# Kernel tuning notes

Measured on AMD Instinct MI355X. Metric: run time of the kernel, lower is better.

The kernel has to match this reference:

```python
import jax, jax.numpy as jnp
import numpy as np

B, T = 128, 100
DZ, DA, DU, K, DOBS, H = 64, 32, 8, 8, 16, 128
JITTER = 1e-4  # _safe_cholesky: sym + jitter*I, then first try adds 1.0*jitter*I again


def setup_inputs() -> dict:
    key = jax.random.key(0)
    ks = jax.random.split(key, 10)
    eye_z = jnp.eye(DZ, dtype=jnp.float32)
    # stable-ish per-component transition matrices
    A_mats = 0.9 * eye_z[None] + 0.05 * jax.random.normal(ks[0], (K, DZ, DZ), jnp.float32)
    B_mats = 0.1 * jax.random.normal(ks[1], (K, DZ, DU), jnp.float32)
    C_mats = 0.3 * jax.random.normal(ks[2], (K, DA, DZ), jnp.float32)
    a_seq = jax.random.normal(ks[3], (B, T, DA), jnp.float32)
    h_obs = jax.random.normal(ks[4], (B, DOBS), jnp.float32)
    u_seq = jax.random.normal(ks[5], (B, T, DU), jnp.float32)
    mask = jnp.ones((B, T), jnp.float32)
    a_0 = jnp.zeros((1, DA), jnp.float32)          # nn.Parameter a_0
    P_0 = 10.0 * eye_z                              # 10 * eye(dim_z)
    Q = 0.05 * eye_z                                # Q_std * eye(dim_z)
    R = 0.05 * jnp.eye(DA, dtype=jnp.float32)       # R_std * eye(dim_a)
    din = DA + DOBS + DU
    s = 1.0 / float(np.sqrt(H))
    W_ih = s * jax.random.normal(ks[6], (3 * H, din), jnp.float32)
    W_hh = s * jax.random.normal(ks[7], (3 * H, H), jnp.float32)
    b_ih = jnp.zeros((3 * H,), jnp.float32)
    b_hh = jnp.zeros((3 * H,), jnp.float32)
    W_out = s * jax.random.normal(ks[8], (K, H), jnp.float32)
    b_out = jnp.zeros((K,), jnp.float32)
    return dict(a_seq=a_seq, h_obs=h_obs, u_seq=u_seq, mask=mask,
                A_mats=A_mats, B_mats=B_mats, C_mats=C_mats,
                a_0=a_0, P_0=P_0, Q=Q, R=R,
                W_ih=W_ih, W_hh=W_hh, b_ih=b_ih, b_hh=b_hh,
                W_out=W_out, b_out=b_out, epoch=100)


def _sym(M):
    return 0.5 * (M + jnp.swapaxes(M, -1, -2))


def _gru_alpha(x, h, W_ih, W_hh, b_ih, b_hh, W_out, b_out):
    # GRU-cell alpha_net: mixture weights over K components
    gi = x @ W_ih.T + b_ih
    gh = h @ W_hh.T + b_hh
    ir, iz, inn = jnp.split(gi, 3, axis=-1)
    hr, hz, hn = jnp.split(gh, 3, axis=-1)
    r = jax.nn.sigmoid(ir + hr)
    zg = jax.nn.sigmoid(iz + hz)
    n = jnp.tanh(inn + r * hn)
    h_new = (1.0 - zg) * n + zg * h
    alpha = jax.nn.softmax(h_new @ W_out.T + b_out, axis=-1)
    return alpha, h_new


def _kalman_forward(a_seq, h_obs, u_seq, mask, A_mats, B_mats, C_mats,
                    a_0, P_0, Q, R, W_ih, W_hh, b_ih, b_hh, W_out, b_out):
    Bsz = a_seq.shape[0]
    I = jnp.eye(DZ, dtype=a_seq.dtype)

    def mix(alpha):
        A = jnp.einsum('bk,kij->bij', alpha, A_mats)
        Bc = jnp.einsum('bk,kij->bij', alpha, B_mats)
        C = jnp.einsum('bk,kij->bij', alpha, C_mats)
        return A, Bc, C

    def alpha_net(a, u, h):
        x = jnp.concatenate([a, h_obs, u], axis=-1)
        return _gru_alpha(x, h, W_ih, W_hh, b_ih, b_hh, W_out, b_out)

    gru_h = jnp.zeros((Bsz, H), a_seq.dtype)
    a_prev = jnp.broadcast_to(a_0, (Bsz, DA))
    alpha0, gru_h = alpha_net(a_prev, u_seq[:, 0], gru_h)
    A_k0, B_k0, C_k0 = mix(alpha0)

    z0 = jnp.zeros((Bsz, DZ), a_seq.dtype)
    P0 = jnp.broadcast_to(P_0, (Bsz, DZ, DZ))

    def step(carry, inp):
        z_prev, P, h, A_k, B_k, C_k = carry
        a_k, u_k, m_k = inp  # [B,da], [B,du], [B]
        mk = m_k[:, None]
        # predict with matrices chosen at previous step
        z = jnp.einsum('bij,bj->bi', A_k, z_prev) + jnp.einsum('bij,bj->bi', B_k, u_k)
        a_hat = jnp.einsum('bij,bj->bi', C_k, z)
        r_k = a_k - a_hat
        CP = jnp.einsum('bij,bjk->bik', C_k, P)                      # C P
        S = jnp.einsum('bik,bjk->bij', CP, C_k) + R                   # C P C^T + R
        # K = solve(S^T, C P^T)^T  (i.e. K = P C^T S^{-1})
        CPt = jnp.einsum('bij,bkj->bik', C_k, P)
        Kg = jnp.swapaxes(jnp.linalg.solve(jnp.swapaxes(S, -1, -2), CPt), -1, -2)
        Kg = Kg * m_k[:, None, None]
        IKC = I - jnp.einsum('bij,bjk->bik', Kg, C_k)
        # Joseph form update
        P_filt = (jnp.einsum('bij,bjk,blk->bil', IKC, P, IKC)
                  + jnp.einsum('bij,jk,blk->bil', Kg, R, Kg))
        P_filt = _sym(P_filt)
        z_mean = z + jnp.einsum('bij,bj->bi', Kg, r_k)
        L = jnp.linalg.cholesky(_sym(P_filt) + 2.0 * JITTER * I)      # safe cholesky
        z_filt = z_mean                                               # dist.mean
        a_filt = jnp.einsum('bij,bj->bi', C_k, z_filt)
        a_k_hat = mk * a_k + (1.0 - mk) * a_filt
        C_old = C_k
        alpha, h = alpha_net(a_k_hat, u_k, h)
        A_n, B_n, C_n = mix(alpha)
        z_pred = (jnp.einsum('bij,bj->bi', A_n, z_filt)
                  + jnp.einsum('bij,bj->bi', B_n, u_k))
        a_pred = jnp.einsum('bij,bj->bi', C_n, z_pred)
        P_pred = _sym(jnp.einsum('bij,bjk,blk->bil', A_n, P_filt, A_n) + Q)
        carry = (z_filt, P_pred, h, A_n, B_n, C_n)
        out = (z_filt, P_filt, z_pred, P_pred, alpha, a_filt, a_pred,
               S, z_mean, L, A_n, B_n, C_old)
        return carry, out

    xs = (jnp.swapaxes(a_seq, 0, 1), jnp.swapaxes(u_seq, 0, 1), jnp.swapaxes(mask, 0, 1))
    _, outs = jax.lax.scan(step, (z0, P0, gru_h, A_k0, B_k0, C_k0), xs)
    # scan outputs are [T, B, ...] -> [B, T, ...]
    (z_filt, P_filt, z_pred, P_pred, alpha_seq, a_filt, a_pred,
     S_pred, z_means, z_scale_tril, A_seq, B_seq, C_seq) = jax.tree.map(
        lambda x: jnp.swapaxes(x, 0, 1), outs)
    return (z_filt, P_filt, z_pred, a_filt, a_pred, P_pred, alpha_seq,
            A_seq, B_seq, C_seq, z_means, z_scale_tril, S_pred)


def reference(a_seq, h_obs, u_seq, mask, A_mats, B_mats, C_mats,
              a_0, P_0, Q, R, W_ih, W_hh, b_ih, b_hh, W_out, b_out, epoch):
    # epoch >= warmup/burn-in thresholds (all 0), so no detach branches apply
    return _kalman_forward(a_seq, h_obs, u_seq, mask, A_mats, B_mats, C_mats,
                           a_0, P_0, Q, R, W_ih, W_hh, b_ih, b_hh, W_out, b_out)
```

## Files before the change

### kernel.cpp

```cpp
#include <hip/hip_runtime.h>

typedef float f4 __attribute__((ext_vector_type(4)));

#define NT 256
#define BB 128
#define BT 100
#define DZc 64
#define DAc 32
#define DUc 8
#define KMIX 8
#define DOBSc 16
#define HG 128
#define DINc 56

#define O_ZFILT   0LL
#define O_PFILT   819200LL
#define O_ZPRED   53248000LL
#define O_AFILT   54067200LL
#define O_APRED   54476800LL
#define O_PPRED   54886400LL
#define O_ALPHA   107315200LL
#define O_ASEQ    107417600LL
#define O_BSEQ    159846400LL
#define O_CSEQ    166400000LL
#define O_ZMEAN   192614400LL
#define O_LTRIL   193433600LL
#define O_SPRED   245862400LL

__device__ __forceinline__ float dot4(f4 a, f4 b) {
    return a[0]*b[0] + a[1]*b[1] + a[2]*b[2] + a[3]*b[3];
}

struct SMem {
    float P[DZc][68];
    float A[DZc][68];
    float AT[DZc][65];
    float Wk[DZc][68];
    float Qm[DZc][68];
    float C[DAc][68];
    float CP[DAc][68];
    float Xm[DAc][68];
    float S[DAc][33];
    float Rm[DAc][33];
    float dinv[DAc];
    float col[64];
    float Bm[DZc][8];
    float z[DZc], zp[DZc], zn[DZc];
    float h[HG], hn[HG];
    float gh[3*HG], gi[3*HG];
    float x[64];
    float ak[DAc], rvec[DAc];
    float u[8];
    float lg[8];
    float mk;
};

template<bool EMIT>
__device__ __forceinline__ void mix_apply(SMem& s, int tid, size_t bt, const float* al8,
    const float* __restrict__ A_mats, const float* __restrict__ B_mats,
    const float* __restrict__ C_mats, float* __restrict__ out)
{
    const f4* A4 = (const f4*)A_mats;
    const f4* B4 = (const f4*)B_mats;
    const f4* C4 = (const f4*)C_mats;
    #pragma unroll 2
    for (int e = 0; e < 4; ++e) {
        int i4 = tid + e*256;
        f4 acc = {0.f,0.f,0.f,0.f};
        #pragma unroll
        for (int k = 0; k < 8; ++k) acc += al8[k] * A4[k*1024 + i4];
        int row = i4 >> 4, cb = (i4 & 15) * 4;
        *(f4*)&s.A[row][cb] = acc;
        s.AT[cb][row] = acc[0]; s.AT[cb+1][row] = acc[1];
        s.AT[cb+2][row] = acc[2]; s.AT[cb+3][row] = acc[3];
        if (EMIT) *(f4*)&out[O_ASEQ + bt*4096 + (size_t)i4*4] = acc;
    }
    if (tid < 128) {
        int i4 = tid;
        f4 acc = {0.f,0.f,0.f,0.f};
        #pragma unroll
        for (int k = 0; k < 8; ++k) acc += al8[k] * B4[k*128 + i4];
        *(f4*)&s.Bm[i4>>1][(i4&1)*4] = acc;
        if (EMIT) *(f4*)&out[O_BSEQ + bt*512 + (size_t)i4*4] = acc;
    }
    #pragma unroll 1
    for (int e = 0; e < 2; ++e) {
        int i4 = tid + e*256;
        f4 acc = {0.f,0.f,0.f,0.f};
        #pragma unroll
        for (int k = 0; k < 8; ++k) acc += al8[k] * C4[k*512 + i4];
        *(f4*)&s.C[i4>>4][(i4&15)*4] = acc;
    }
}

__global__ void __launch_bounds__(NT, 1)
kalman_seq(const float* __restrict__ a_seq, const float* __restrict__ h_obs,
           const float* __restrict__ u_seq, const float* __restrict__ mask,
           const float* __restrict__ A_mats, const float* __restrict__ B_mats,
           const float* __restrict__ C_mats, const float* __restrict__ a_0,
           const float* __restrict__ P_0, const float* __restrict__ Q,
           const float* __restrict__ R, const float* __restrict__ W_ih,
           const float* __restrict__ W_hh, const float* __restrict__ b_ih,
           const float* __restrict__ b_hh, const float* __restrict__ W_out,
           const float* __restrict__ b_out, float* __restrict__ out)
{
    __shared__ SMem s;
    const int b = blockIdx.x;
    const int tid = threadIdx.x;
    const int r4 = (tid >> 4) << 2;
    const int c4 = (tid & 15) << 2;

    for (int idx = tid; idx < DZc*DZc; idx += NT) {
        s.P[idx >> 6][idx & 63]  = P_0[idx];
        s.Qm[idx >> 6][idx & 63] = Q[idx];
    }
    for (int idx = tid; idx < DAc*DAc; idx += NT) s.Rm[idx >> 5][idx & 31] = R[idx];
    if (tid < HG) s.h[tid] = 0.f;
    if (tid < DZc) s.z[tid] = 0.f;
    if (tid < DAc)                 s.x[tid] = a_0[tid];
    else if (tid < DAc + DOBSc)    s.x[tid] = h_obs[b*DOBSc + (tid - DAc)];
    else if (tid < DINc)           s.x[tid] = u_seq[(size_t)b*BT*DUc + (tid - DAc - DOBSc)];
    __syncthreads();

    for (int g = tid; g < 3*HG; g += NT) {
        const float* wi = W_ih + (size_t)g * DINc;
        f4 ai = {0.f,0.f,0.f,0.f};
        #pragma unroll 7
        for (int q = 0; q < 14; ++q) ai += *(const f4*)(wi + q*4) * *(const f4*)&s.x[q*4];
        s.gi[g] = ai[0]+ai[1]+ai[2]+ai[3] + b_ih[g];
        s.gh[g] = b_hh[g];
    }
    __syncthreads();
    if (tid < HG) {
        float r  = 1.f / (1.f + expf(-(s.gi[tid] + s.gh[tid])));
        float zg = 1.f / (1.f + expf(-(s.gi[HG+tid] + s.gh[HG+tid])));
        float n  = tanhf(s.gi[2*HG+tid] + r * s.gh[2*HG+tid]);
        s.h[tid] = (1.f - zg) * n;
    }
    __syncthreads();
    if (tid < KMIX) {
        const float* wo = W_out + tid * HG;
        f4 acc = {0.f,0.f,0.f,0.f};
        #pragma unroll 8
        for (int q = 0; q < 32; ++q) acc += *(const f4*)(wo + q*4) * *(const f4*)&s.h[q*4];
        s.lg[tid] = acc[0]+acc[1]+acc[2]+acc[3] + b_out[tid];
    }
    __syncthreads();
    {
        float lg[8];
        #pragma unroll
        for (int k = 0; k < 8; ++k) lg[k] = s.lg[k];
        float mx = lg[0];
        #pragma unroll
        for (int k = 1; k < 8; ++k) mx = fmaxf(mx, lg[k]);
        float al[8]; float sum = 0.f;
        #pragma unroll
        for (int k = 0; k < 8; ++k) { al[k] = expf(lg[k] - mx); sum += al[k]; }
        float rs = 1.f / sum;
        #pragma unroll
        for (int k = 0; k < 8; ++k) al[k] *= rs;
        mix_apply<false>(s, tid, 0, al, A_mats, B_mats, C_mats, out);
    }
    __syncthreads();

    for (int t = 0; t < BT; ++t) {
        const size_t bt = (size_t)b * BT + t;

        if (tid < 64) {
            float acc = 0.f;
            #pragma unroll 8
            for (int k = 0; k < DZc; ++k) acc += s.AT[k][tid] * s.z[k];
            const float* up = u_seq + bt*DUc;
            #pragma unroll
            for (int q = 0; q < DUc; ++q) acc += s.Bm[tid][q] * up[q];
            s.zp[tid] = acc;
        } else if (tid < 96) {
            float av = a_seq[bt*DAc + (tid-64)];
            s.ak[tid-64] = av;
            s.x[tid-64] = av;
        } else if (tid < 104) {
            float uv = u_seq[bt*DUc + (tid-96)];
            s.u[tid-96] = uv; s.x[48 + (tid-96)] = uv;
        } else if (tid == 104) {
            s.mk = mask[bt];
        }
        __syncthreads();
        const float mkv = s.mk;
        const bool mk1 = (mkv == 1.0f);

        {
            const int r = tid >> 3;
            const int c8 = (tid & 7) * 8;
            f4 acc0 = {0.f,0.f,0.f,0.f}, acc1 = {0.f,0.f,0.f,0.f};
            #pragma unroll 4
            for (int k4 = 0; k4 < 16; ++k4) {
                f4 cr = *(const f4*)&s.C[r][k4*4];
                #pragma unroll
                for (int kk = 0; kk < 4; ++kk) {
                    float cv = cr[kk];
                    acc0 += cv * *(const f4*)&s.P[k4*4+kk][c8];
                    acc1 += cv * *(const f4*)&s.P[k4*4+kk][c8+4];
                }
            }
            *(f4*)&s.CP[r][c8]   = acc0;
            *(f4*)&s.CP[r][c8+4] = acc1;
        }
        if (tid < DAc) {
            float acc = 0.f;
            #pragma unroll 4
            for (int k4 = 0; k4 < 16; ++k4)
                acc += dot4(*(const f4*)&s.C[tid][k4*4], *(const f4*)&s.zp[k4*4]);
            s.rvec[tid] = s.ak[tid] - acc;
        }
        __syncthreads();

        {
            const int r = tid >> 3;
            const int cb = (tid & 7) * 4;
            f4 acc = {0.f,0.f,0.f,0.f};
            #pragma unroll 4
            for (int k4 = 0; k4 < 16; ++k4) {
                f4 a = *(const f4*)&s.CP[r][k4*4];
                #pragma unroll
                for (int j = 0; j < 4; ++j)
                    acc[j] += dot4(a, *(const f4*)&s.C[cb+j][k4*4]);
            }
            f4 rm = {s.Rm[r][cb], s.Rm[r][cb+1], s.Rm[r][cb+2], s.Rm[r][cb+3]};
            f4 v = acc + rm;
            s.S[r][cb] = v[0]; s.S[r][cb+1] = v[1]; s.S[r][cb+2] = v[2]; s.S[r][cb+3] = v[3];
            *(f4*)&out[O_SPRED + bt*1024 + (size_t)r*32 + cb] = v;
        }
        __syncthreads();

        if (tid < 64) {
            const int lane = tid;
            const int l = lane & 31;
            float row[32];
            #pragma unroll
            for (int j = 0; j < 32; ++j) row[j] = s.S[l][j];
            #pragma unroll
            for (int k = 0; k < 32; ++k) {
                if (lane < 32) s.col[lane] = row[k];
                __threadfence_block();
                float cb[32];
                #pragma unroll
                for (int jv = 0; jv < 8; ++jv) {
                    if (jv*4 + 3 >= k) {
                        f4 cv = *(const f4*)&s.col[jv*4];
                        cb[jv*4] = cv[0]; cb[jv*4+1] = cv[1];
                        cb[jv*4+2] = cv[2]; cb[jv*4+3] = cv[3];
                    }
                }
                float dv = 1.0f / cb[k];
                if (lane == k) s.dinv[k] = dv;
                float fm = (l > k) ? (row[k] * dv) : 0.f;
                #pragma unroll
                for (int j = k+1; j < 32; ++j)
                    row[j] -= fm * cb[j];
                __threadfence_block();
            }
            if (lane < 32) {
                #pragma unroll
                for (int j = 0; j < 32; ++j) s.S[l][j] = row[j];
            }
            __threadfence_block();
            float v[32];
            #pragma unroll
            for (int r = 0; r < 32; ++r) v[r] = s.CP[r][lane];
            #pragma unroll
            for (int r = 0; r < 32; ++r) {
                float acc = v[r];
                #pragma unroll
                for (int k = 0; k < r; ++k) acc -= s.S[r][k] * v[k];
                v[r] = s.dinv[r] * acc;
            }
            #pragma unroll
            for (int r = 30; r >= 0; --r) {
                float acc = 0.f;
                #pragma unroll
                for (int k = r+1; k < 32; ++k) acc += s.S[k][r] * v[k];
                v[r] -= s.dinv[r] * acc;
            }
            float accz = 0.f;
            #pragma unroll
            for (int r = 0; r < 32; ++r) {
                s.Xm[r][lane] = v[r];
                accz += v[r] * s.rvec[r];
            }
            s.zn[lane] = s.zp[lane] + mkv * accz;
            __threadfence_block();
            if (lane < DAc) {
                float acc = 0.f;
                #pragma unroll 4
                for (int k4 = 0; k4 < 16; ++k4)
                    acc += dot4(*(const f4*)&s.C[lane][k4*4], *(const f4*)&s.zn[k4*4]);
                out[O_AFILT + bt*DAc + lane] = acc;
                if (!mk1) s.x[lane] = mkv * s.ak[lane] + (1.f - mkv) * acc;
            }
        } else if (tid < 192) {
            const int idx = tid - 64;
            const float* wir = W_ih + (size_t)idx * DINc;
            const float* wiz = W_ih + (size_t)(HG + idx) * DINc;
            const float* win = W_ih + (size_t)(2*HG + idx) * DINc;
            const float* whr = W_hh + (size_t)idx * HG;
            const float* whz = W_hh + (size_t)(HG + idx) * HG;
            const float* whn = W_hh + (size_t)(2*HG + idx) * HG;
            f4 air = {0.f,0.f,0.f,0.f}, aiz = {0.f,0.f,0.f,0.f}, ain = {0.f,0.f,0.f,0.f};
            #pragma unroll 4
            for (int q = 0; q < 14; ++q) {
                f4 xv = *(const f4*)&s.x[q*4];
                air += *(const f4*)(wir + q*4) * xv;
                aiz += *(const f4*)(wiz + q*4) * xv;
                ain += *(const f4*)(win + q*4) * xv;
            }
            f4 ahr = {0.f,0.f,0.f,0.f}, ahz = {0.f,0.f,0.f,0.f}, ahn = {0.f,0.f,0.f,0.f};
            #pragma unroll 4
            for (int q = 0; q < 32; ++q) {
                f4 hv = *(const f4*)&s.h[q*4];
                ahr += *(const f4*)(whr + q*4) * hv;
                ahz += *(const f4*)(whz + q*4) * hv;
                ahn += *(const f4*)(whn + q*4) * hv;
            }
            float gir = air[0]+air[1]+air[2]+air[3] + b_ih[idx];
            float giz = aiz[0]+aiz[1]+aiz[2]+aiz[3] + b_ih[HG + idx];
            float gin = ain[0]+ain[1]+ain[2]+ain[3] + b_ih[2*HG + idx];
            float ghr = ahr[0]+ahr[1]+ahr[2]+ahr[3] + b_hh[idx];
            float ghz = ahz[0]+ahz[1]+ahz[2]+ahz[3] + b_hh[HG + idx];
            float ghn = ahn[0]+ahn[1]+ahn[2]+ahn[3] + b_hh[2*HG + idx];
            float r  = 1.f / (1.f + expf(-(gir + ghr)));
            float zg = 1.f / (1.f + expf(-(giz + ghz)));
            float n  = tanhf(gin + r * ghn);
            s.hn[idx] = (1.f - zg) * n + zg * s.h[idx];
        } else {
            const int l = tid - 192;
            #pragma unroll 2
            for (int e = 0; e < 8; ++e) {
                int i4 = l + e*64;
                *(f4*)&out[O_CSEQ + bt*2048 + (size_t)i4*4] = *(const f4*)&s.C[i4>>4][(i4&15)*4];
            }
        }
        __syncthreads();

        {
            const float coef = (mkv*mkv - 2.f*mkv) * 0.5f;
            f4 acc0 = {0.f,0.f,0.f,0.f}, acc1 = {0.f,0.f,0.f,0.f};
            f4 acc2 = {0.f,0.f,0.f,0.f}, acc3 = {0.f,0.f,0.f,0.f};
            #pragma unroll 4
            for (int l = 0; l < DAc; ++l) {
                f4 cpc = *(const f4*)&s.CP[l][c4];
                f4 xc  = *(const f4*)&s.Xm[l][c4];
                f4 cpr = *(const f4*)&s.CP[l][r4];
                f4 xr  = *(const f4*)&s.Xm[l][r4];
                acc0 += xr[0]*cpc + cpr[0]*xc;
                acc1 += xr[1]*cpc + cpr[1]*xc;
                acc2 += xr[2]*cpc + cpr[2]*xc;
                acc3 += xr[3]*cpc + cpr[3]*xc;
            }
            #pragma unroll
            for (int i = 0; i < 4; ++i) {
                const int row = r4 + i;
                f4 g = (i==0) ? acc0 : (i==1) ? acc1 : (i==2) ? acc2 : acc3;
                f4 p = *(const f4*)&s.P[row][c4];
                f4 v = p + coef * g;
                *(f4*)&s.P[row][c4] = v;
                *(f4*)&out[O_PFILT + bt*4096 + (size_t)row*64 + c4] = v;
            }
        }
        if (tid < DZc) {
            float v = s.zn[tid];
            out[O_ZFILT + bt*DZc + tid] = v;
            out[O_ZMEAN + bt*DZc + tid] = v;
            s.z[tid] = v;
        }

        if (!mk1) {
            __syncthreads();
            for (int g = tid; g < 3*HG; g += NT) {
                const float* wi = W_ih + (size_t)g * DINc;
                const float* wh = W_hh + (size_t)g * HG;
                f4 ai = {0.f,0.f,0.f,0.f}, ah = {0.f,0.f,0.f,0.f};
                #pragma unroll 7
                for (int q = 0; q < 14; ++q) ai += *(const f4*)(wi + q*4) * *(const f4*)&s.x[q*4];
                #pragma unroll 8
                for (int q = 0; q < 32; ++q) ah += *(const f4*)(wh + q*4) * *(const f4*)&s.h[q*4];
                s.gi[g] = ai[0]+ai[1]+ai[2]+ai[3] + b_ih[g];
                s.gh[g] = ah[0]+ah[1]+ah[2]+ah[3] + b_hh[g];
            }
            __syncthreads();
            if (tid < HG) {
                float gi0 = s.gi[tid], gi1 = s.gi[HG+tid], gi2 = s.gi[2*HG+tid];
                float gh0 = s.gh[tid], gh1 = s.gh[HG+tid], gh2 = s.gh[2*HG+tid];
                float hold = s.h[tid];
                float r  = 1.f / (1.f + expf(-(gi0 + gh0)));
                float zg = 1.f / (1.f + expf(-(gi1 + gh1)));
                float n  = tanhf(gi2 + r * gh2);
                s.hn[tid] = (1.f - zg) * n + zg * hold;
            }
            __syncthreads();
        }

        {
            const int lane = tid & 63;
            const int g = lane >> 3;
            const int cb = (lane & 7) * 16;
            f4 a4 = {0.f,0.f,0.f,0.f};
            #pragma unroll
            for (int q = 0; q < 4; ++q)
                a4 += *(const f4*)(W_out + (size_t)g*HG + cb + q*4) * *(const f4*)&s.hn[cb + q*4];
            float acc = a4[0]+a4[1]+a4[2]+a4[3];
            acc += __shfl_xor(acc, 1); acc += __shfl_xor(acc, 2); acc += __shfl_xor(acc, 4);
            float lg[8];
            #pragma unroll
            for (int k = 0; k < 8; ++k) lg[k] = __shfl(acc, k*8) + b_out[k];
            float mx = lg[0];
            #pragma unroll
            for (int k = 1; k < 8; ++k) mx = fmaxf(mx, lg[k]);
            float al[8]; float sum = 0.f;
            #pragma unroll
            for (int k = 0; k < 8; ++k) { al[k] = expf(lg[k] - mx); sum += al[k]; }
            float rs = 1.f / sum;
            #pragma unroll
            for (int k = 0; k < 8; ++k) al[k] *= rs;
            if (tid < 8) out[O_ALPHA + bt*8 + tid] = al[tid];
            mix_apply<true>(s, tid, bt, al, A_mats, B_mats, C_mats, out);
        }
        if (tid < HG) s.h[tid] = s.hn[tid];
        __syncthreads();

        if (tid < 64) {
            float acc = 0.f;
            #pragma unroll 8
            for (int k = 0; k < DZc; ++k) acc += s.AT[k][tid] * s.z[k];
            acc += dot4(*(const f4*)&s.Bm[tid][0], *(const f4*)&s.u[0]);
            acc += dot4(*(const f4*)&s.Bm[tid][4], *(const f4*)&s.u[4]);
            s.zp[tid] = acc;
            out[O_ZPRED + bt*DZc + tid] = acc;
        }
        {
            f4 acc[4] = {{0.f,0.f,0.f,0.f},{0.f,0.f,0.f,0.f},{0.f,0.f,0.f,0.f},{0.f,0.f,0.f,0.f}};
            #pragma unroll 2
            for (int k4 = 0; k4 < 16; ++k4) {
                f4 ar0 = *(const f4*)&s.A[r4+0][k4*4];
                f4 ar1 = *(const f4*)&s.A[r4+1][k4*4];
                f4 ar2 = *(const f4*)&s.A[r4+2][k4*4];
                f4 ar3 = *(const f4*)&s.A[r4+3][k4*4];
                #pragma unroll
                for (int kk = 0; kk < 4; ++kk) {
                    f4 bv = *(const f4*)&s.P[k4*4+kk][c4];
                    acc[0] += ar0[kk] * bv; acc[1] += ar1[kk] * bv;
                    acc[2] += ar2[kk] * bv; acc[3] += ar3[kk] * bv;
                }
            }
            #pragma unroll
            for (int i = 0; i < 4; ++i)
                *(f4*)&s.Wk[r4+i][c4] = acc[i];
        }
        __syncthreads();

        {
            f4 acc[4] = {{0.f,0.f,0.f,0.f},{0.f,0.f,0.f,0.f},{0.f,0.f,0.f,0.f},{0.f,0.f,0.f,0.f}};
            #pragma unroll 2
            for (int k4 = 0; k4 < 16; ++k4) {
                f4 w0 = *(const f4*)&s.Wk[r4+0][k4*4];
                f4 w1 = *(const f4*)&s.Wk[r4+1][k4*4];
                f4 w2 = *(const f4*)&s.Wk[r4+2][k4*4];
                f4 w3 = *(const f4*)&s.Wk[r4+3][k4*4];
                #pragma unroll
                for (int kk = 0; kk < 4; ++kk) {
                    f4 av = *(const f4*)&s.AT[k4*4+kk][c4];
                    acc[0] += w0[kk] * av; acc[1] += w1[kk] * av;
                    acc[2] += w2[kk] * av; acc[3] += w3[kk] * av;
                }
            }
            #pragma unroll
            for (int i = 0; i < 4; ++i) {
                const int row = r4 + i;
                f4 q = *(const f4*)&s.Qm[row][c4];
                f4 v = acc[i] + q;
                *(f4*)&s.P[row][c4] = v;
                *(f4*)&out[O_PPRED + bt*4096 + (size_t)row*64 + c4] = v;
            }
        }
        if (tid < DAc) {
            float acc = 0.f;
            #pragma unroll 4
            for (int k4 = 0; k4 < 16; ++k4)
                acc += dot4(*(const f4*)&s.C[tid][k4*4], *(const f4*)&s.zp[k4*4]);
            out[O_APRED + bt*DAc + tid] = acc;
        }
        __syncthreads();
    }
}

__global__ void __launch_bounds__(64)
chol_batch(float* __restrict__ out)
{
    __shared__ float M[DZc][65];
    __shared__ float sd[DZc];
    const size_t bt = blockIdx.x;
    const int lane = threadIdx.x;
    const float* src = out + O_PFILT + bt*4096;
    #pragma unroll 4
    for (int e = 0; e < 16; ++e) {
        int i4 = lane + e*64;
        f4 v = *(const f4*)(src + (size_t)i4*4);
        int row = i4 >> 4, cb = (i4 & 15) * 4;
        M[row][cb] = v[0]; M[row][cb+1] = v[1]; M[row][cb+2] = v[2]; M[row][cb+3] = v[3];
    }
    __syncthreads();
    M[lane][lane] += 2.0e-4f;
    __syncthreads();
    for (int k = 0; k < DZc; ++k) {
        __threadfence_block();
        float mkk = M[k][k];
        if (lane == k) sd[k] = sqrtf(mkk);
        if (lane > k) {
            float f = M[lane][k] / mkk;
            for (int j = k + 1; j <= lane; ++j)
                M[lane][j] -= f * M[j][k];
        }
    }
    __threadfence_block();
    for (int k = 0; k < lane; ++k) M[lane][k] /= sd[k];
    M[lane][lane] = sd[lane];
    for (int k = lane + 1; k < DZc; ++k) M[lane][k] = 0.f;
    __syncthreads();
    float* dst = out + O_LTRIL + bt*4096;
    #pragma unroll 4
    for (int e = 0; e < 16; ++e) {
        int i4 = lane + e*64;
        int row = i4 >> 4, cb = (i4 & 15) * 4;
        f4 v = {M[row][cb], M[row][cb+1], M[row][cb+2], M[row][cb+3]};
        *(f4*)(dst + (size_t)i4*4) = v;
    }
}

extern "C" void kernel_launch(void* const* d_in, const int* in_sizes, int n_in,
                              void* d_out, int out_size, void* d_ws, size_t ws_size,
                              hipStream_t stream) {
    const float* a_seq  = (const float*)d_in[0];
    const float* h_obs  = (const float*)d_in[1];
    const float* u_seq  = (const float*)d_in[2];
    const float* mask   = (const float*)d_in[3];
    const float* A_mats = (const float*)d_in[4];
    const float* B_mats = (const float*)d_in[5];
    const float* C_mats = (const float*)d_in[6];
    const float* a_0    = (const float*)d_in[7];
    const float* P_0    = (const float*)d_in[8];
    const float* Q      = (const float*)d_in[9];
    const float* R      = (const float*)d_in[10];
    const float* W_ih   = (const float*)d_in[11];
    const float* W_hh   = (const float*)d_in[12];
    const float* b_ih   = (const float*)d_in[13];
    const float* b_hh   = (const float*)d_in[14];
    const float* W_out  = (const float*)d_in[15];
    const float* b_out  = (const float*)d_in[16];
    float* out = (float*)d_out;

    kalman_seq<<<dim3(BB), dim3(NT), 0, stream>>>(a_seq, h_obs, u_seq, mask,
        A_mats, B_mats, C_mats, a_0, P_0, Q, R, W_ih, W_hh, b_ih, b_hh, W_out, b_out, out);
    chol_batch<<<dim3(BB*BT), dim3(64), 0, stream>>>(out);
}
```

Measured before the change: 6.457 ms.

## Prefetch next-step inputs, reuse predicted state, and shuffle-based Cholesky pivots

Loads a_seq, u_seq and mask for step t+1 into registers partway through step t and stores them into double-buffered shared slots, which takes global-load latency off the start of each step. The step-start prediction now reuses the previously computed zp and corrects only the control term using the difference between consecutive u values, so the 64-length A·z dot product is no longer recomputed. The in-loop 32x32 LU/Cholesky factorization broadcasts pivot rows with warp shuffles instead of a shared-memory column and fences. The zp reuse changes floating-point summation order slightly, and correctness depends on zp and ubuf being initialised consistently at t=0.

```diff
diff --git a/kernel.cpp b/kernel.cpp
--- a/kernel.cpp
+++ b/kernel.cpp
@@ -43,14 +43,15 @@
     float S[DAc][33];
     float Rm[DAc][33];
     float dinv[DAc];
-    float col[64];
     float Bm[DZc][8];
     float z[DZc], zp[DZc], zn[DZc];
     float h[HG], hn[HG];
     float gh[3*HG], gi[3*HG];
     float x[64];
     float ak[DAc], rvec[DAc];
-    float u[8];
+    float akN[DAc];
+    float ubuf[2][8];
+    float mkN;
     float lg[8];
     float mk;
 };
@@ -116,10 +117,14 @@
     }
     for (int idx = tid; idx < DAc*DAc; idx += NT) s.Rm[idx >> 5][idx & 31] = R[idx];
     if (tid < HG) s.h[tid] = 0.f;
-    if (tid < DZc) s.z[tid] = 0.f;
+    if (tid < DZc) { s.z[tid] = 0.f; s.zp[tid] = 0.f; }
     if (tid < DAc)                 s.x[tid] = a_0[tid];
     else if (tid < DAc + DOBSc)    s.x[tid] = h_obs[b*DOBSc + (tid - DAc)];
     else if (tid < DINc)           s.x[tid] = u_seq[(size_t)b*BT*DUc + (tid - DAc - DOBSc)];
+    if (tid >= 128 && tid < 160)      s.akN[tid-128] = a_seq[(size_t)b*BT*DAc + (tid-128)];
+    else if (tid >= 160 && tid < 168) { s.ubuf[0][tid-160] = u_seq[(size_t)b*BT*DUc + (tid-160)];
+                                        s.ubuf[1][tid-160] = 0.f; }
+    else if (tid == 168)              s.mkN = mask[(size_t)b*BT];
     __syncthreads();
 
     for (int g = tid; g < 3*HG; g += NT) {
@@ -165,24 +170,22 @@
 
     for (int t = 0; t < BT; ++t) {
         const size_t bt = (size_t)b * BT + t;
+        const int cur = t & 1;
 
         if (tid < 64) {
-            float acc = 0.f;
-            #pragma unroll 8
-            for (int k = 0; k < DZc; ++k) acc += s.AT[k][tid] * s.z[k];
-            const float* up = u_seq + bt*DUc;
-            #pragma unroll
-            for (int q = 0; q < DUc; ++q) acc += s.Bm[tid][q] * up[q];
+            float acc = s.zp[tid];
+            #pragma unroll
+            for (int q = 0; q < DUc; ++q)
+                acc += s.Bm[tid][q] * (s.ubuf[cur][q] - s.ubuf[cur^1][q]);
             s.zp[tid] = acc;
         } else if (tid < 96) {
-            float av = a_seq[bt*DAc + (tid-64)];
+            float av = s.akN[tid-64];
             s.ak[tid-64] = av;
             s.x[tid-64] = av;
         } else if (tid < 104) {
-            float uv = u_seq[bt*DUc + (tid-96)];
-            s.u[tid-96] = uv; s.x[48 + (tid-96)] = uv;
+            s.x[48 + (tid-96)] = s.ubuf[cur][tid-96];
         } else if (tid == 104) {
-            s.mk = mask[bt];
+            s.mk = s.mkN;
         }
         __syncthreads();
         const float mkv = s.mk;
@@ -240,24 +243,13 @@
             for (int j = 0; j < 32; ++j) row[j] = s.S[l][j];
             #pragma unroll
             for (int k = 0; k < 32; ++k) {
-                if (lane < 32) s.col[lane] = row[k];
-                __threadfence_block();
-                float cb[32];
-                #pragma unroll
-                for (int jv = 0; jv < 8; ++jv) {
-                    if (jv*4 + 3 >= k) {
-                        f4 cv = *(const f4*)&s.col[jv*4];
-                        cb[jv*4] = cv[0]; cb[jv*4+1] = cv[1];
-                        cb[jv*4+2] = cv[2]; cb[jv*4+3] = cv[3];
-                    }
-                }
-                float dv = 1.0f / cb[k];
+                float piv = __shfl(row[k], k);
+                float dv = 1.0f / piv;
                 if (lane == k) s.dinv[k] = dv;
                 float fm = (l > k) ? (row[k] * dv) : 0.f;
                 #pragma unroll
                 for (int j = k+1; j < 32; ++j)
-                    row[j] -= fm * cb[j];
-                __threadfence_block();
+                    row[j] -= fm * __shfl(row[k], j);
             }
             if (lane < 32) {
                 #pragma unroll
@@ -341,6 +333,15 @@
         }
         __syncthreads();
 
+        float pfA = 0.f, pfU = 0.f, pfM = 0.f;
+        {
+            const int t2 = (t+1 < BT) ? (t+1) : t;
+            const size_t bt2 = (size_t)b*BT + t2;
+            if (tid >= 192 && tid < 224)      pfA = a_seq[bt2*DAc + (tid-192)];
+            else if (tid >= 224 && tid < 232) pfU = u_seq[bt2*DUc + (tid-224)];
+            else if (tid == 232)              pfM = mask[bt2];
+        }
+
         {
             const float coef = (mkv*mkv - 2.f*mkv) * 0.5f;
             f4 acc0 = {0.f,0.f,0.f,0.f}, acc1 = {0.f,0.f,0.f,0.f};
@@ -431,8 +432,8 @@
             float acc = 0.f;
             #pragma unroll 8
             for (int k = 0; k < DZc; ++k) acc += s.AT[k][tid] * s.z[k];
-            acc += dot4(*(const f4*)&s.Bm[tid][0], *(const f4*)&s.u[0]);
-            acc += dot4(*(const f4*)&s.Bm[tid][4], *(const f4*)&s.u[4]);
+            #pragma unroll
+            for (int q = 0; q < DUc; ++q) acc += s.Bm[tid][q] * s.ubuf[cur][q];
             s.zp[tid] = acc;
             out[O_ZPRED + bt*DZc + tid] = acc;
         }
@@ -488,6 +489,9 @@
                 acc += dot4(*(const f4*)&s.C[tid][k4*4], *(const f4*)&s.zp[k4*4]);
             out[O_APRED + bt*DAc + tid] = acc;
         }
+        if (tid >= 192 && tid < 224)      s.akN[tid-192] = pfA;
+        else if (tid >= 224 && tid < 232) s.ubuf[(t+1)&1][tid-224] = pfU;
+        else if (tid == 232)              s.mkN = pfM;
         __syncthreads();
     }
 }
```

Result: slower. 8.152 ms (+26.2%).
